# Optimization experiments

Hardware: AMD Instinct MI355X
Metric: run time of the kernel (lower is better)

## Reference

```python
import jax, jax.numpy as jnp
import numpy as np

N, F_IN, H, C, E, K = 100000, 128, 512, 16, 3200000, 3
EPS = 1e-5


def setup_inputs() -> dict:
    key = jax.random.key(0)
    ks = jax.random.split(key, 12)
    x = jax.random.normal(ks[0], (N, F_IN), jnp.float32)
    edge_index = jax.random.randint(ks[1], (2, E), 0, N, jnp.int64)
    # TAGConv has K+1 hop linears (bias folded into one vector, like PyG)
    W1 = jax.random.normal(ks[2], (K + 1, F_IN, H), jnp.float32) * 0.02
    b1 = jnp.zeros((H,), jnp.float32)
    W2 = jax.random.normal(ks[3], (K + 1, H, H), jnp.float32) * 0.02
    b2 = jnp.zeros((H,), jnp.float32)
    W3 = jax.random.normal(ks[4], (K + 1, H, C), jnp.float32) * 0.02
    b3 = jnp.zeros((C,), jnp.float32)
    gn1_w = jnp.ones((H,), jnp.float32)
    gn1_b = jnp.zeros((H,), jnp.float32)
    gn1_a = jnp.ones((H,), jnp.float32)  # mean_scale alpha
    gn2_w = jnp.ones((H,), jnp.float32)
    gn2_b = jnp.zeros((H,), jnp.float32)
    gn2_a = jnp.ones((H,), jnp.float32)
    return {"x": x, "edge_index": edge_index,
            "W1": W1, "b1": b1, "W2": W2, "b2": b2, "W3": W3, "b3": b3,
            "gn1_w": gn1_w, "gn1_b": gn1_b, "gn1_a": gn1_a,
            "gn2_w": gn2_w, "gn2_b": gn2_b, "gn2_a": gn2_a}


def _gcn_norm(edge_index, n):
    # PyG TAGConv: gcn_norm with add_self_loops=False, all-ones edge weights
    row, col = edge_index[0], edge_index[1]  # source j, target i
    deg = jax.ops.segment_sum(jnp.ones((edge_index.shape[1],), jnp.float32), col,
                              num_segments=n)
    dinv = jnp.where(deg > 0, jax.lax.rsqrt(jnp.maximum(deg, 1.0)), 0.0)
    return row, col, dinv[row] * dinv[col]


def _prop(h, row, col, norm, n):
    # out[i] = sum_{(j->i)} norm_e * h[j]
    return jax.ops.segment_sum(norm[:, None] * h[row], col, num_segments=n)


def _tagconv(x, row, col, norm, W, b):
    n = x.shape[0]
    out = x @ W[0]
    h = x
    for k in range(1, W.shape[0]):
        h = _prop(h, row, col, norm, n)
        out = out + h @ W[k]
    return out + b


def _graphnorm(x, w, b, a):
    # single graph: per-graph mean/var over all nodes
    mean = jnp.mean(x, axis=0)
    sub = x - a * mean
    var = jnp.mean(sub * sub, axis=0)
    return sub * jax.lax.rsqrt(var + EPS) * w + b


def reference(x, edge_index, W1, b1, W2, b2, W3, b3,
              gn1_w, gn1_b, gn1_a, gn2_w, gn2_b, gn2_a):
    n = x.shape[0]
    row, col, norm = _gcn_norm(edge_index, n)
    h = jax.nn.relu(_tagconv(x, row, col, norm, W1, b1))
    h = _graphnorm(h, gn1_w, gn1_b, gn1_a)
    h = jax.nn.relu(_tagconv(h, row, col, norm, W2, b2))
    h = _graphnorm(h, gn2_w, gn2_b, gn2_a)
    return _tagconv(h, row, col, norm, W3, b3)
```

## Files before the change

### kernel.cpp

```cpp
#include <hip/hip_runtime.h>

#define NN 100000
#define EE 3200000
#define EPSF 1e-5f

typedef unsigned short u16;
typedef short bf16x8 __attribute__((ext_vector_type(8)));
typedef float f32x4 __attribute__((ext_vector_type(4)));

static inline int cdiv(int a, int b) { return (a + b - 1) / b; }

__device__ __forceinline__ float b2f(u16 u) {
    return __uint_as_float((unsigned int)u << 16);
}
__device__ __forceinline__ u16 f2b(float f) {
    unsigned int i = __float_as_uint(f);
    return (u16)((i + 0x7FFFu + ((i >> 16) & 1u)) >> 16);
}
__device__ __forceinline__ int ep_src(unsigned int p) { return (int)(p & 0x1FFFFu); }
__device__ __forceinline__ float ep_w(unsigned int p) {
    return __uint_as_float(p & 0xFFFE0000u);
}
__device__ __forceinline__ unsigned pkhi(float f0, float f1) {
    return __builtin_amdgcn_perm(__float_as_uint(f1), __float_as_uint(f0), 0x07060302u);
}

__global__ void k_init(int* __restrict__ deg, int* __restrict__ cursor,
                       float* __restrict__ stats) {
    int i = blockIdx.x * 256 + threadIdx.x;
    if (i < NN) {
        deg[i] = 0;
        cursor[i] = 0;
    }
    if (i < 2048) stats[i] = 0.f;
}

__global__ void k_deg(const int* __restrict__ col, int* __restrict__ deg) {
    int i = blockIdx.x * 256 + threadIdx.x;
    if (i < EE) atomicAdd(&deg[col[i]], 1);
}

__global__ void k_dinv(const int* __restrict__ deg, float* __restrict__ dinv) {
    int i = blockIdx.x * 256 + threadIdx.x;
    if (i < NN) {
        int d = deg[i];
        dinv[i] = d > 0 ? rsqrtf((float)d) : 0.f;
    }
}

__global__ void k_scan(const int* __restrict__ deg, int* __restrict__ offs) {
    __shared__ int sh[1024];
    int tid = threadIdx.x;
    int start = tid * 98;
    int end = min(start + 98, NN);
    int sum = 0;
    for (int i = start; i < end; ++i) sum += deg[i];
    sh[tid] = sum;
    __syncthreads();
    for (int off = 1; off < 1024; off <<= 1) {
        int t = (tid >= off) ? sh[tid - off] : 0;
        __syncthreads();
        sh[tid] += t;
        __syncthreads();
    }
    int base = tid ? sh[tid - 1] : 0;
    for (int i = start; i < end; ++i) {
        offs[i] = base;
        base += deg[i];
    }
    if (tid == 1023) offs[NN] = sh[1023];
}

__global__ void k_scatter(const int* __restrict__ row, const int* __restrict__ col,
                          const float* __restrict__ dinv, const int* __restrict__ offs,
                          int* __restrict__ cursor, unsigned int* __restrict__ ep) {
    int i = blockIdx.x * 256 + threadIdx.x;
    if (i < EE) {
        int c = col[i], r = row[i];
        int pos = offs[c] + atomicAdd(&cursor[c], 1);
        float w = dinv[r] * dinv[c];
        unsigned int u = __float_as_uint(w);
        unsigned int rb = (u + 0xFFFFu + ((u >> 17) & 1u)) & 0xFFFE0000u;
        ep[pos] = rb | (unsigned int)r;
    }
}

__global__ void k_cvt(const float* __restrict__ src, u16* __restrict__ dst, int n4) {
    int idx = blockIdx.x * 256 + threadIdx.x;
    if (idx >= n4) return;
    float4 v = ((const float4*)src)[idx];
    ushort4 o;
    o.x = f2b(v.x);
    o.y = f2b(v.y);
    o.z = f2b(v.z);
    o.w = f2b(v.w);
    ((ushort4*)dst)[idx] = o;
}

__global__ void k_cvt8s(const u16* __restrict__ src, int lds_, unsigned char* __restrict__ dst,
                        int ldd) {
    int idx = blockIdx.x * 256 + threadIdx.x;
    if (idx >= NN * 128) return;
    int node = idx >> 7, f2 = (idx & 127) << 1;
    ushort2 v = *(const ushort2*)(src + (size_t)node * lds_ + f2);
    int pk = __builtin_amdgcn_cvt_pk_fp8_f32(b2f(v.x), b2f(v.y), 0, false);
    uchar2 o;
    o.x = (unsigned char)(pk & 0xFF);
    o.y = (unsigned char)((pk >> 8) & 0xFF);
    *(uchar2*)(dst + (size_t)node * ldd + f2) = o;
}

template <int S8>
__global__ void k_prop_t(const void* __restrict__ in, int ldin,
                         unsigned char* __restrict__ out8, int ldo8,
                         const int* __restrict__ offs, const unsigned int* __restrict__ ep) {
    int node = blockIdx.x;
    int f2 = threadIdx.x << 1;
    int s = offs[node], e = offs[node + 1];
    const u16* inb = (const u16*)in;
    const unsigned char* in8 = (const unsigned char*)in;
    float a0 = 0.f, a1 = 0.f;
    int t = s;
    for (; t + 4 <= e; t += 4) {
        unsigned int p0 = ep[t], p1 = ep[t + 1], p2 = ep[t + 2], p3 = ep[t + 3];
        float x0, y0, x1, y1, x2, y2, x3, y3;
        if (S8) {
            uchar2 c0 = *(const uchar2*)(in8 + (size_t)ep_src(p0) * ldin + f2);
            uchar2 c1 = *(const uchar2*)(in8 + (size_t)ep_src(p1) * ldin + f2);
            uchar2 c2 = *(const uchar2*)(in8 + (size_t)ep_src(p2) * ldin + f2);
            uchar2 c3 = *(const uchar2*)(in8 + (size_t)ep_src(p3) * ldin + f2);
            int w0 = c0.x | (c0.y << 8), w1 = c1.x | (c1.y << 8);
            int w2 = c2.x | (c2.y << 8), w3 = c3.x | (c3.y << 8);
            x0 = __builtin_amdgcn_cvt_f32_fp8(w0, 0);
            y0 = __builtin_amdgcn_cvt_f32_fp8(w0, 1);
            x1 = __builtin_amdgcn_cvt_f32_fp8(w1, 0);
            y1 = __builtin_amdgcn_cvt_f32_fp8(w1, 1);
            x2 = __builtin_amdgcn_cvt_f32_fp8(w2, 0);
            y2 = __builtin_amdgcn_cvt_f32_fp8(w2, 1);
            x3 = __builtin_amdgcn_cvt_f32_fp8(w3, 0);
            y3 = __builtin_amdgcn_cvt_f32_fp8(w3, 1);
        } else {
            ushort2 v0 = *(const ushort2*)(inb + (size_t)ep_src(p0) * ldin + f2);
            ushort2 v1 = *(const ushort2*)(inb + (size_t)ep_src(p1) * ldin + f2);
            ushort2 v2 = *(const ushort2*)(inb + (size_t)ep_src(p2) * ldin + f2);
            ushort2 v3 = *(const ushort2*)(inb + (size_t)ep_src(p3) * ldin + f2);
            x0 = b2f(v0.x);
            y0 = b2f(v0.y);
            x1 = b2f(v1.x);
            y1 = b2f(v1.y);
            x2 = b2f(v2.x);
            y2 = b2f(v2.y);
            x3 = b2f(v3.x);
            y3 = b2f(v3.y);
        }
        float w0 = ep_w(p0), w1 = ep_w(p1), w2 = ep_w(p2), w3 = ep_w(p3);
        a0 = fmaf(w0, x0, a0);
        a1 = fmaf(w0, y0, a1);
        a0 = fmaf(w1, x1, a0);
        a1 = fmaf(w1, y1, a1);
        a0 = fmaf(w2, x2, a0);
        a1 = fmaf(w2, y2, a1);
        a0 = fmaf(w3, x3, a0);
        a1 = fmaf(w3, y3, a1);
    }
    for (; t < e; ++t) {
        unsigned int p0 = ep[t];
        float x0, y0;
        if (S8) {
            uchar2 c0 = *(const uchar2*)(in8 + (size_t)ep_src(p0) * ldin + f2);
            int w = c0.x | (c0.y << 8);
            x0 = __builtin_amdgcn_cvt_f32_fp8(w, 0);
            y0 = __builtin_amdgcn_cvt_f32_fp8(w, 1);
        } else {
            ushort2 v0 = *(const ushort2*)(inb + (size_t)ep_src(p0) * ldin + f2);
            x0 = b2f(v0.x);
            y0 = b2f(v0.y);
        }
        float w0 = ep_w(p0);
        a0 = fmaf(w0, x0, a0);
        a1 = fmaf(w0, y0, a1);
    }
    int pk = __builtin_amdgcn_cvt_pk_fp8_f32(a0, a1, 0, false);
    uchar2 o8;
    o8.x = (unsigned char)(pk & 0xFF);
    o8.y = (unsigned char)((pk >> 8) & 0xFF);
    *(uchar2*)(out8 + (size_t)node * ldo8 + f2) = o8;
}

__global__ void k_prop256(const unsigned char* __restrict__ in, int ldin,
                          unsigned char* __restrict__ out, int ldout,
                          const int* __restrict__ offs, const unsigned int* __restrict__ ep) {
    int node = blockIdx.x;
    int f4 = threadIdx.x << 2;
    int s = offs[node], e = offs[node + 1];
    float a0 = 0, a1 = 0, a2 = 0, a3 = 0;
    int t = s;
    for (; t + 4 <= e; t += 4) {
        unsigned int p[4];
        unsigned int v[4];
#pragma unroll
        for (int u = 0; u < 4; ++u) p[u] = ep[t + u];
#pragma unroll
        for (int u = 0; u < 4; ++u)
            v[u] = *(const unsigned int*)(in + (size_t)ep_src(p[u]) * ldin + f4);
#pragma unroll
        for (int u = 0; u < 4; ++u) {
            float w = ep_w(p[u]);
            a0 = fmaf(w, __builtin_amdgcn_cvt_f32_fp8((int)v[u], 0), a0);
            a1 = fmaf(w, __builtin_amdgcn_cvt_f32_fp8((int)v[u], 1), a1);
            a2 = fmaf(w, __builtin_amdgcn_cvt_f32_fp8((int)v[u], 2), a2);
            a3 = fmaf(w, __builtin_amdgcn_cvt_f32_fp8((int)v[u], 3), a3);
        }
    }
    for (; t < e; ++t) {
        unsigned int p0 = ep[t];
        unsigned int v = *(const unsigned int*)(in + (size_t)ep_src(p0) * ldin + f4);
        float w = ep_w(p0);
        a0 = fmaf(w, __builtin_amdgcn_cvt_f32_fp8((int)v, 0), a0);
        a1 = fmaf(w, __builtin_amdgcn_cvt_f32_fp8((int)v, 1), a1);
        a2 = fmaf(w, __builtin_amdgcn_cvt_f32_fp8((int)v, 2), a2);
        a3 = fmaf(w, __builtin_amdgcn_cvt_f32_fp8((int)v, 3), a3);
    }
    int p01 = __builtin_amdgcn_cvt_pk_fp8_f32(a0, a1, 0, false);
    int p23 = __builtin_amdgcn_cvt_pk_fp8_f32(a2, a3, 0, false);
    unsigned int o = (unsigned)(p01 & 0xFFFF) | ((unsigned)p23 << 16);
    *(unsigned int*)(out + (size_t)node * ldout + f4) = o;
}

__global__ void k_prop16(const float* __restrict__ in, int ldin,
                         const float* __restrict__ add, int ldadd,
                         float* __restrict__ out, const float* __restrict__ bias,
                         const int* __restrict__ offs, const unsigned int* __restrict__ ep) {
    int node = blockIdx.x * 16 + (threadIdx.x >> 4);
    if (node >= NN) return;
    int f = threadIdx.x & 15;
    float acc = add[(size_t)node * ldadd + f];
    int s = offs[node], e = offs[node + 1];
    int t = s;
    for (; t + 8 <= e; t += 8) {
        unsigned int p[8];
        float v[8];
#pragma unroll
        for (int u = 0; u < 8; ++u) p[u] = ep[t + u];
#pragma unroll
        for (int u = 0; u < 8; ++u) v[u] = in[(size_t)ep_src(p[u]) * ldin + f];
#pragma unroll
        for (int u = 0; u < 8; ++u) acc = fmaf(ep_w(p[u]), v[u], acc);
    }
    for (; t < e; ++t) {
        unsigned int p0 = ep[t];
        acc = fmaf(ep_w(p0), in[(size_t)ep_src(p0) * ldin + f], acc);
    }
    if (bias) acc += bias[f];
    out[node * 16 + f] = acc;
}

__global__ __launch_bounds__(256, 4) void k_gemm_mfma(
    const void* __restrict__ A0, int lda0, const void* __restrict__ A1, int lda1,
    const void* __restrict__ A2, int lda2, const void* __restrict__ A3, int lda3, int a8mask,
    const u16* __restrict__ B0, const u16* __restrict__ B1, const u16* __restrict__ B2,
    const u16* __restrict__ B3, int ldb, void* __restrict__ Cv, int ldc, int M, int Ncols,
    int Ktot, int Kq, const float* __restrict__ bias, int relu, int cmode,
    float* __restrict__ statsOut) {
    __shared__ __align__(16) char AsB[2][8192];
    __shared__ __align__(16) char BsB[2][8192];
    __shared__ float sstat[256];
    int tid = threadIdx.x;
    int wave = tid >> 6, lane = tid & 63;
    int quad = lane >> 4, lq = lane & 15;
    int wr = wave >> 1, wc = wave & 1;
    int gx = gridDim.x;
    int nwg = gx * (int)gridDim.y;
    int lin = blockIdx.y * gx + blockIdx.x;
    int xcd = lin & 7, kk8 = lin >> 3;
    int q8 = nwg >> 3, r8 = nwg & 7;
    int wgid = (xcd < r8 ? xcd * (q8 + 1) : r8 * (q8 + 1) + (xcd - r8) * q8) + kk8;
    int m0 = (wgid / gx) * 128, n0 = (wgid % gx) * 128;
    int r = tid >> 1, h = tid & 1;
    int gr = m0 + r;
    if (gr > M - 1) gr = M - 1;
    f32x4 acc[4][4] = {};
    if (statsOut) sstat[tid] = 0.f;

    const int NT = Ktot >> 5;
    const int spm = (Kq >> 5) - 1;
    const int sps = __popc(spm);

    auto loadA = [&](int u, uint4& x0, uint4& x1, int& t8) {
        int sU = u < NT ? u : NT - 1;
        int src = sU >> sps, kk = (sU & spm) << 5;
        const char* Ap = (const char*)(src == 0 ? A0 : src == 1 ? A1 : src == 2 ? A2 : A3);
        int lda = src == 0 ? lda0 : src == 1 ? lda1 : src == 2 ? lda2 : lda3;
        t8 = (a8mask >> src) & 1;
        if (t8) {
            x0 = *(const uint4*)(Ap + (size_t)gr * lda + kk + h * 16);
        } else {
            const char* base = Ap + (size_t)gr * ((size_t)lda * 2) + (size_t)kk * 2 + h * 32;
            x0 = *(const uint4*)base;
            x1 = *(const uint4*)(base + 16);
        }
    };
    auto writeA = [&](int buf, uint4 x0, uint4 x1, int t8) {
        uint4 lo, hi;
        if (t8) {
            lo.x = pkhi(__builtin_amdgcn_cvt_f32_fp8((int)x0.x, 0),
                        __builtin_amdgcn_cvt_f32_fp8((int)x0.x, 1));
            lo.y = pkhi(__builtin_amdgcn_cvt_f32_fp8((int)x0.x, 2),
                        __builtin_amdgcn_cvt_f32_fp8((int)x0.x, 3));
            lo.z = pkhi(__builtin_amdgcn_cvt_f32_fp8((int)x0.y, 0),
                        __builtin_amdgcn_cvt_f32_fp8((int)x0.y, 1));
            lo.w = pkhi(__builtin_amdgcn_cvt_f32_fp8((int)x0.y, 2),
                        __builtin_amdgcn_cvt_f32_fp8((int)x0.y, 3));
            hi.x = pkhi(__builtin_amdgcn_cvt_f32_fp8((int)x0.z, 0),
                        __builtin_amdgcn_cvt_f32_fp8((int)x0.z, 1));
            hi.y = pkhi(__builtin_amdgcn_cvt_f32_fp8((int)x0.z, 2),
                        __builtin_amdgcn_cvt_f32_fp8((int)x0.z, 3));
            hi.z = pkhi(__builtin_amdgcn_cvt_f32_fp8((int)x0.w, 0),
                        __builtin_amdgcn_cvt_f32_fp8((int)x0.w, 1));
            hi.w = pkhi(__builtin_amdgcn_cvt_f32_fp8((int)x0.w, 2),
                        __builtin_amdgcn_cvt_f32_fp8((int)x0.w, 3));
        } else {
            lo = x0;
            hi = x1;
        }
        int s = ((r >> 1) & 3) << 4;
        char* dst = AsB[buf] + r * 64;
        *(uint4*)(dst + ((h * 32) ^ s)) = lo;
        *(uint4*)(dst + ((h * 32 + 16) ^ s)) = hi;
    };
    auto stageB = [&](int buf, int u) {
        int sU = u < NT ? u : NT - 1;
        int src = sU >> sps, kk = (sU & spm) << 5;
        const u16* Bp = src == 0 ? B0 : src == 1 ? B1 : src == 2 ? B2 : B3;
#pragma unroll
        for (int i = 0; i < 2; ++i) {
            int L = i * 4096 + wave * 1024 + lane * 16;
            int rr = L >> 6;
            int kog = (L & 63) ^ (((rr >> 1) & 3) << 4);
            int gn = n0 + rr;
            if (gn > Ncols - 1) gn = Ncols - 1;
            const char* g = (const char*)Bp + (size_t)gn * ((size_t)ldb * 2) +
                            (size_t)kk * 2 + kog;
            __builtin_amdgcn_global_load_lds(
                (const __attribute__((address_space(1))) void*)g,
                (__attribute__((address_space(3))) void*)(BsB[buf] + i * 4096 + wave * 1024),
                16, 0, 0);
        }
    };

    uint4 pa0, pa1;
    int pt8;
    {
        uint4 a0_, a1_;
        int t8_;
        loadA(0, a0_, a1_, t8_);
        stageB(0, 0);
        asm volatile("s_waitcnt vmcnt(2)" ::: "memory");
        __builtin_amdgcn_sched_barrier(0);
        writeA(0, a0_, a1_, t8_);
        loadA(1, pa0, pa1, pt8);
        if (pt8)
            asm volatile("s_waitcnt vmcnt(1) lgkmcnt(0)" ::: "memory");
        else
            asm volatile("s_waitcnt vmcnt(2) lgkmcnt(0)" ::: "memory");
        __builtin_amdgcn_sched_barrier(0);
        __builtin_amdgcn_s_barrier();
    }

    int cur = 0;
    for (int t = 0; t < NT; ++t) {
        int nxt = cur ^ 1;
        stageB(nxt, t + 1);
        const char* Ac = AsB[cur];
        const char* Bc = BsB[cur];
        bf16x8 af[4], bfr[4];
#pragma unroll
        for (int i = 0; i < 4; ++i) {
            int rr = wr * 64 + i * 16 + lq;
            af[i] = *(const bf16x8*)(Ac + rr * 64 + ((quad * 16) ^ (((rr >> 1) & 3) << 4)));
        }
#pragma unroll
        for (int j = 0; j < 4; ++j) {
            int nn2 = wc * 64 + j * 16 + lq;
            bfr[j] = *(const bf16x8*)(Bc + nn2 * 64 + ((quad * 16) ^ (((nn2 >> 1) & 3) << 4)));
        }
#pragma unroll
        for (int i = 0; i < 4; ++i)
#pragma unroll
            for (int j = 0; j < 4; ++j)
                acc[i][j] = __builtin_amdgcn_mfma_f32_16x16x32_bf16(af[i], bfr[j], acc[i][j],
                                                                    0, 0, 0);
        asm volatile("s_waitcnt vmcnt(2)" ::: "memory");
        __builtin_amdgcn_sched_barrier(0);
        writeA(nxt, pa0, pa1, pt8);
        loadA(t + 2, pa0, pa1, pt8);
        if (pt8)
            asm volatile("s_waitcnt vmcnt(1) lgkmcnt(0)" ::: "memory");
        else
            asm volatile("s_waitcnt vmcnt(2) lgkmcnt(0)" ::: "memory");
        __builtin_amdgcn_sched_barrier(0);
        __builtin_amdgcn_s_barrier();
        cur = nxt;
    }

#pragma unroll
    for (int i = 0; i < 4; ++i) {
#pragma unroll
        for (int j = 0; j < 4; ++j) {
            int jc = wc * 64 + j * 16 + lq;
            int c = n0 + jc;
            bool cok = c < Ncols;
            float bcol = (bias && cok) ? bias[c] : 0.f;
            int rbase = m0 + wr * 64 + i * 16 + quad * 4;
            float ls = 0.f, lq2 = 0.f;
#pragma unroll
            for (int reg = 0; reg < 4; ++reg) {
                int rr = rbase + reg;
                if (rr >= M || !cok) continue;
                float t = acc[i][j][reg];
                if (cmode == 2) t += b2f(*((u16*)Cv + (size_t)rr * ldc + c));
                t += bcol;
                if (relu) t = fmaxf(t, 0.f);
                if (cmode == 0)
                    ((float*)Cv)[(size_t)rr * ldc + c] = t;
                else
                    *((u16*)Cv + (size_t)rr * ldc + c) = f2b(t);
                ls += t;
                lq2 += t * t;
            }
            if (statsOut && cok) {
                atomicAdd(&sstat[jc], ls);
                atomicAdd(&sstat[128 + jc], lq2);
            }
        }
    }
    if (statsOut) {
        __syncthreads();
        if (tid < 128)
            atomicAdd(&statsOut[n0 + tid], sstat[tid]);
        else
            atomicAdd(&statsOut[512 + n0 + (tid - 128)], sstat[tid]);
    }
}

__global__ void k_gnorm(u16* __restrict__ X, int ld, const float* __restrict__ stats,
                        const float* __restrict__ w, const float* __restrict__ b,
                        const float* __restrict__ a) {
    int i = blockIdx.x;
    int c = threadIdx.x * 2;
    const float invn = 1.f / NN;
    ushort2 v = *(ushort2*)(X + (size_t)i * ld + c);
    float x0 = b2f(v.x), x1 = b2f(v.y);
    {
        float m = stats[c] * invn, q = stats[512 + c] * invn, al = a[c];
        float var = q - (2.f * al - al * al) * m * m;
        x0 = (x0 - al * m) * rsqrtf(var + EPSF) * w[c] + b[c];
    }
    {
        int c1 = c + 1;
        float m = stats[c1] * invn, q = stats[512 + c1] * invn, al = a[c1];
        float var = q - (2.f * al - al * al) * m * m;
        x1 = (x1 - al * m) * rsqrtf(var + EPSF) * w[c1] + b[c1];
    }
    v.x = f2b(x0);
    v.y = f2b(x1);
    *(ushort2*)(X + (size_t)i * ld + c) = v;
}

__global__ void k_wt(const float* __restrict__ src, u16* __restrict__ dst, int I, int O,
                     int total) {
    int idx = blockIdx.x * 256 + threadIdx.x;
    if (idx >= total) return;
    int io = I * O;
    int k = idx / io, rem = idx - k * io;
    int n = rem / I, i = rem - n * I;
    dst[idx] = f2b(src[(size_t)k * io + (size_t)i * O + n]);
}

__global__ void k_wt3(const float* __restrict__ W3, u16* __restrict__ W3T) {
    int idx = blockIdx.x * 256 + threadIdx.x;
    if (idx >= 64 * 512) return;
    int n = idx >> 9, i = idx & 511;
    int k = n >> 4, f = n & 15;
    W3T[idx] = f2b(W3[((size_t)k * 512 + i) * 16 + f]);
}

extern "C" void kernel_launch(void* const* d_in, const int* in_sizes, int n_in,
                              void* d_out, int out_size, void* d_ws, size_t ws_size,
                              hipStream_t stream) {
    const float* x = (const float*)d_in[0];
    const int* ei = (const int*)d_in[1];
    const float* W1 = (const float*)d_in[2];
    const float* b1 = (const float*)d_in[3];
    const float* W2 = (const float*)d_in[4];
    const float* b2 = (const float*)d_in[5];
    const float* W3 = (const float*)d_in[6];
    const float* b3 = (const float*)d_in[7];
    const float* g1w = (const float*)d_in[8];
    const float* g1b = (const float*)d_in[9];
    const float* g1a = (const float*)d_in[10];
    const float* g2w = (const float*)d_in[11];
    const float* g2b = (const float*)d_in[12];
    const float* g2a = (const float*)d_in[13];
    const int* row = ei;
    const int* col = ei + EE;

    char* p = (char*)d_ws;
    auto alloc = [&](size_t bytes) {
        char* r = p;
        p += (bytes + 255) & ~(size_t)255;
        return r;
    };
    u16* H1 = (u16*)alloc((size_t)NN * 512 * 2);
    u16* Y = (u16*)alloc((size_t)NN * 512 * 2);
    unsigned char* X8 = (unsigned char*)alloc((size_t)NN * 256);
    unsigned int* ep = (unsigned int*)alloc((size_t)EE * 4);
    u16* W1T = (u16*)alloc((size_t)4 * 512 * 128 * 2);
    u16* W2T = (u16*)alloc((size_t)4 * 512 * 512 * 2);
    u16* W3T = (u16*)alloc(64 * 512 * 2);
    float* dinv = (float*)alloc((size_t)NN * 4);
    float* stats = (float*)alloc(2048 * 4);
    int* deg = (int*)alloc((size_t)NN * 4);
    int* offs = (int*)alloc((size_t)(NN + 1) * 4);
    int* cursor = (int*)alloc((size_t)NN * 4);
    (void)ws_size;
    (void)in_sizes;
    (void)n_in;
    (void)out_size;

    u16* xb = Y;
    unsigned char* F8a = (unsigned char*)Y + (size_t)NN * 256;
    unsigned char* F8b = (unsigned char*)Y + (size_t)NN * 256 + (size_t)NN * 128;

    k_init<<<cdiv(NN, 256), 256, 0, stream>>>(deg, cursor, stats);
    k_deg<<<cdiv(EE, 256), 256, 0, stream>>>(col, deg);
    k_dinv<<<cdiv(NN, 256), 256, 0, stream>>>(deg, dinv);
    k_scan<<<1, 1024, 0, stream>>>(deg, offs);
    k_scatter<<<cdiv(EE, 256), 256, 0, stream>>>(row, col, dinv, offs, cursor, ep);
    k_wt<<<cdiv(4 * 128 * 512, 256), 256, 0, stream>>>(W1, W1T, 128, 512, 4 * 128 * 512);
    k_wt<<<cdiv(4 * 512 * 512, 256), 256, 0, stream>>>(W2, W2T, 512, 512, 4 * 512 * 512);
    k_wt3<<<cdiv(64 * 512, 256), 256, 0, stream>>>(W3, W3T);

    dim3 gg(512 / 128, cdiv(NN, 128));
    const size_t WQ = (size_t)512 * 512;
    const size_t W1Q = (size_t)512 * 128;

    k_cvt<<<cdiv(NN * 32, 256), 256, 0, stream>>>(x, xb, NN * 32);
    k_prop_t<0><<<NN, 64, 0, stream>>>(xb, 128, F8a, 128, offs, ep);
    k_prop_t<1><<<NN, 64, 0, stream>>>(F8a, 128, F8b, 128, offs, ep);
    k_prop_t<1><<<NN, 64, 0, stream>>>(F8b, 128, X8, 128, offs, ep);
    k_gemm_mfma<<<gg, 256, 0, stream>>>(xb, 128, F8a, 128, F8b, 128, X8, 128, 14, W1T,
                                        W1T + W1Q, W1T + 2 * W1Q, W1T + 3 * W1Q, 128, H1, 512,
                                        NN, 512, 512, 128, b1, 1, 1, stats);
    k_gnorm<<<NN, 256, 0, stream>>>(H1, 512, stats, g1w, g1b, g1a);

    unsigned char* hpA = (unsigned char*)H1;
    unsigned char* hpB = (unsigned char*)H1 + 256;
    {
        u16* h1c0 = H1;
        k_cvt8s<<<cdiv(NN * 128, 256), 256, 0, stream>>>(h1c0, 512, X8, 256);
        k_gemm_mfma<<<gg, 256, 0, stream>>>(h1c0, 512, h1c0, 512, h1c0, 512, h1c0, 512, 0,
                                            W2T, W2T, W2T, W2T, 512, Y, 512, NN, 512, 256,
                                            256, nullptr, 0, 1, nullptr);
        k_prop256<<<NN, 64, 0, stream>>>(X8, 256, hpA, 1024, offs, ep);
        k_prop256<<<NN, 64, 0, stream>>>(hpA, 1024, hpB, 1024, offs, ep);
        k_prop256<<<NN, 64, 0, stream>>>(hpB, 1024, X8, 256, offs, ep);
        k_gemm_mfma<<<gg, 256, 0, stream>>>(hpA, 1024, hpB, 1024, X8, 256, X8, 256, 7,
                                            W2T + WQ, W2T + 2 * WQ, W2T + 3 * WQ, W2T, 512,
                                            Y, 512, NN, 512, 768, 256, nullptr, 0, 2,
                                            nullptr);
    }
    {
        u16* h1c1 = H1 + 256;
        k_cvt8s<<<cdiv(NN * 128, 256), 256, 0, stream>>>(h1c1, 512, X8, 256);
        k_prop256<<<NN, 64, 0, stream>>>(X8, 256, hpA, 1024, offs, ep);
        k_prop256<<<NN, 64, 0, stream>>>(hpA, 1024, hpB, 1024, offs, ep);
        k_prop256<<<NN, 64, 0, stream>>>(hpB, 1024, X8, 256, offs, ep);
        k_gemm_mfma<<<gg, 256, 0, stream>>>(h1c1, 512, hpA, 1024, hpB, 1024, X8, 256, 14,
                                            W2T + 256, W2T + WQ + 256, W2T + 2 * WQ + 256,
                                            W2T + 3 * WQ + 256, 512, Y, 512, NN, 512, 1024,
                                            256, b2, 1, 2, stats + 1024);
    }
    k_gnorm<<<NN, 256, 0, stream>>>(Y, 512, stats + 1024, g2w, g2b, g2a);

    float* G = (float*)H1;
    float* tA = (float*)X8;
    float* tB = tA + (size_t)NN * 16;
    {
        dim3 g3(1, cdiv(NN, 128));
        k_gemm_mfma<<<g3, 256, 0, stream>>>(Y, 512, Y, 512, Y, 512, Y, 512, 0, W3T, W3T, W3T,
                                            W3T, 512, G, 64, NN, 64, 512, 512, nullptr, 0, 0,
                                            nullptr);
    }
    k_prop16<<<cdiv(NN, 16), 256, 0, stream>>>(G + 48, 64, G + 32, 64, tA, nullptr, offs, ep);
    k_prop16<<<cdiv(NN, 16), 256, 0, stream>>>(tA, 16, G + 16, 64, tB, nullptr, offs, ep);
    k_prop16<<<cdiv(NN, 16), 256, 0, stream>>>(tB, 16, G + 0, 64, (float*)d_out, b3, offs, ep);
}
```

Measured before the change: 2.988 ms.

## Deepen A-operand prefetch to two tiles and drop XCD-aware block remap

Restructures the MFMA GEMM main loop to prefetch A tiles two iterations ahead, unrolling by two with fixed register sets so that the vmcnt waits are uniform. FP8 A loads are split into two 8-byte loads so that both the FP8 and bf16 paths issue two loads each, and the FP8 write layout is changed to match. The XCD-aware workgroup remapping is removed in favour of plain blockIdx tiling, and launch bounds are lowered to 3 waves per SIMD to leave room for the extra prefetch registers. The deeper prefetch is meant to hide global load latency. In exchange it costs occupancy and L2 locality, and the unrolled loop assumes an even tile count NT.

```diff
diff --git a/kernel.cpp b/kernel.cpp
--- a/kernel.cpp
+++ b/kernel.cpp
@@ -255,7 +255,7 @@
     out[node * 16 + f] = acc;
 }
 
-__global__ __launch_bounds__(256, 4) void k_gemm_mfma(
+__global__ __launch_bounds__(256, 3) void k_gemm_mfma(
     const void* __restrict__ A0, int lda0, const void* __restrict__ A1, int lda1,
     const void* __restrict__ A2, int lda2, const void* __restrict__ A3, int lda3, int a8mask,
     const u16* __restrict__ B0, const u16* __restrict__ B1, const u16* __restrict__ B2,
@@ -269,13 +269,7 @@
     int wave = tid >> 6, lane = tid & 63;
     int quad = lane >> 4, lq = lane & 15;
     int wr = wave >> 1, wc = wave & 1;
-    int gx = gridDim.x;
-    int nwg = gx * (int)gridDim.y;
-    int lin = blockIdx.y * gx + blockIdx.x;
-    int xcd = lin & 7, kk8 = lin >> 3;
-    int q8 = nwg >> 3, r8 = nwg & 7;
-    int wgid = (xcd < r8 ? xcd * (q8 + 1) : r8 * (q8 + 1) + (xcd - r8) * q8) + kk8;
-    int m0 = (wgid / gx) * 128, n0 = (wgid % gx) * 128;
+    int m0 = blockIdx.y * 128, n0 = blockIdx.x * 128;
     int r = tid >> 1, h = tid & 1;
     int gr = m0 + r;
     if (gr > M - 1) gr = M - 1;
@@ -293,7 +287,13 @@
         int lda = src == 0 ? lda0 : src == 1 ? lda1 : src == 2 ? lda2 : lda3;
         t8 = (a8mask >> src) & 1;
         if (t8) {
-            x0 = *(const uint4*)(Ap + (size_t)gr * lda + kk + h * 16);
+            const char* base = Ap + (size_t)gr * lda + kk;
+            uint2 a = *(const uint2*)(base + h * 8);
+            uint2 b = *(const uint2*)(base + 16 + h * 8);
+            x0.x = a.x;
+            x0.y = a.y;
+            x1.x = b.x;
+            x1.y = b.y;
         } else {
             const char* base = Ap + (size_t)gr * ((size_t)lda * 2) + (size_t)kk * 2 + h * 32;
             x0 = *(const uint4*)base;
@@ -301,8 +301,10 @@
         }
     };
     auto writeA = [&](int buf, uint4 x0, uint4 x1, int t8) {
-        uint4 lo, hi;
+        int s = ((r >> 1) & 3) << 4;
+        char* dst = AsB[buf] + r * 64;
         if (t8) {
+            uint4 lo, hi;
             lo.x = pkhi(__builtin_amdgcn_cvt_f32_fp8((int)x0.x, 0),
                         __builtin_amdgcn_cvt_f32_fp8((int)x0.x, 1));
             lo.y = pkhi(__builtin_amdgcn_cvt_f32_fp8((int)x0.x, 2),
@@ -311,22 +313,20 @@
                         __builtin_amdgcn_cvt_f32_fp8((int)x0.y, 1));
             lo.w = pkhi(__builtin_amdgcn_cvt_f32_fp8((int)x0.y, 2),
                         __builtin_amdgcn_cvt_f32_fp8((int)x0.y, 3));
-            hi.x = pkhi(__builtin_amdgcn_cvt_f32_fp8((int)x0.z, 0),
-                        __builtin_amdgcn_cvt_f32_fp8((int)x0.z, 1));
-            hi.y = pkhi(__builtin_amdgcn_cvt_f32_fp8((int)x0.z, 2),
-                        __builtin_amdgcn_cvt_f32_fp8((int)x0.z, 3));
-            hi.z = pkhi(__builtin_amdgcn_cvt_f32_fp8((int)x0.w, 0),
-                        __builtin_amdgcn_cvt_f32_fp8((int)x0.w, 1));
-            hi.w = pkhi(__builtin_amdgcn_cvt_f32_fp8((int)x0.w, 2),
-                        __builtin_amdgcn_cvt_f32_fp8((int)x0.w, 3));
+            hi.x = pkhi(__builtin_amdgcn_cvt_f32_fp8((int)x1.x, 0),
+                        __builtin_amdgcn_cvt_f32_fp8((int)x1.x, 1));
+            hi.y = pkhi(__builtin_amdgcn_cvt_f32_fp8((int)x1.x, 2),
+                        __builtin_amdgcn_cvt_f32_fp8((int)x1.x, 3));
+            hi.z = pkhi(__builtin_amdgcn_cvt_f32_fp8((int)x1.y, 0),
+                        __builtin_amdgcn_cvt_f32_fp8((int)x1.y, 1));
+            hi.w = pkhi(__builtin_amdgcn_cvt_f32_fp8((int)x1.y, 2),
+                        __builtin_amdgcn_cvt_f32_fp8((int)x1.y, 3));
+            *(uint4*)(dst + ((h * 16) ^ s)) = lo;
+            *(uint4*)(dst + ((32 + h * 16) ^ s)) = hi;
         } else {
-            lo = x0;
-            hi = x1;
-        }
-        int s = ((r >> 1) & 3) << 4;
-        char* dst = AsB[buf] + r * 64;
-        *(uint4*)(dst + ((h * 32) ^ s)) = lo;
-        *(uint4*)(dst + ((h * 32 + 16) ^ s)) = hi;
+            *(uint4*)(dst + ((h * 32) ^ s)) = x0;
+            *(uint4*)(dst + ((h * 32 + 16) ^ s)) = x1;
+        }
     };
     auto stageB = [&](int buf, int u) {
         int sU = u < NT ? u : NT - 1;
@@ -347,32 +347,9 @@
                 16, 0, 0);
         }
     };
-
-    uint4 pa0, pa1;
-    int pt8;
-    {
-        uint4 a0_, a1_;
-        int t8_;
-        loadA(0, a0_, a1_, t8_);
-        stageB(0, 0);
-        asm volatile("s_waitcnt vmcnt(2)" ::: "memory");
-        __builtin_amdgcn_sched_barrier(0);
-        writeA(0, a0_, a1_, t8_);
-        loadA(1, pa0, pa1, pt8);
-        if (pt8)
-            asm volatile("s_waitcnt vmcnt(1) lgkmcnt(0)" ::: "memory");
-        else
-            asm volatile("s_waitcnt vmcnt(2) lgkmcnt(0)" ::: "memory");
-        __builtin_amdgcn_sched_barrier(0);
-        __builtin_amdgcn_s_barrier();
-    }
-
-    int cur = 0;
-    for (int t = 0; t < NT; ++t) {
-        int nxt = cur ^ 1;
-        stageB(nxt, t + 1);
-        const char* Ac = AsB[cur];
-        const char* Bc = BsB[cur];
+    auto compute = [&](int bufc) {
+        const char* Ac = AsB[bufc];
+        const char* Bc = BsB[bufc];
         bf16x8 af[4], bfr[4];
 #pragma unroll
         for (int i = 0; i < 4; ++i) {
@@ -390,17 +367,48 @@
             for (int j = 0; j < 4; ++j)
                 acc[i][j] = __builtin_amdgcn_mfma_f32_16x16x32_bf16(af[i], bfr[j], acc[i][j],
                                                                     0, 0, 0);
-        asm volatile("s_waitcnt vmcnt(2)" ::: "memory");
+    };
+
+    uint4 wAx, wAy, wBx, wBy;
+    int wA8, wB8;
+    {
+        uint4 a0x, a0y;
+        int a08;
+        loadA(0, a0x, a0y, a08);
+        stageB(0, 0);
+        loadA(1, wAx, wAy, wA8);
+        loadA(2, wBx, wBy, wB8);
+        asm volatile("s_waitcnt vmcnt(4)" ::: "memory");
         __builtin_amdgcn_sched_barrier(0);
-        writeA(nxt, pa0, pa1, pt8);
-        loadA(t + 2, pa0, pa1, pt8);
-        if (pt8)
-            asm volatile("s_waitcnt vmcnt(1) lgkmcnt(0)" ::: "memory");
-        else
-            asm volatile("s_waitcnt vmcnt(2) lgkmcnt(0)" ::: "memory");
+        writeA(0, a0x, a0y, a08);
+        asm volatile("s_waitcnt lgkmcnt(0)" ::: "memory");
         __builtin_amdgcn_sched_barrier(0);
         __builtin_amdgcn_s_barrier();
-        cur = nxt;
+    }
+
+    for (int t = 0; t < NT; t += 2) {
+        {
+            stageB(1, t + 1);
+            compute(0);
+            asm volatile("s_waitcnt vmcnt(4)" ::: "memory");
+            __builtin_amdgcn_sched_barrier(0);
+            writeA(1, wAx, wAy, wA8);
+            loadA(t + 3, wAx, wAy, wA8);
+            asm volatile("s_waitcnt vmcnt(2) lgkmcnt(0)" ::: "memory");
+            __builtin_amdgcn_sched_barrier(0);
+            __builtin_amdgcn_s_barrier();
+        }
+        {
+            stageB(0, t + 2);
+            compute(1);
+            asm volatile("s_waitcnt vmcnt(4)" ::: "memory");
+            __builtin_amdgcn_sched_barrier(0);
+            writeA(0, wBx, wBy, wB8);
+            loadA(t + 4, wBx, wBy, wB8);
+            asm volatile("s_waitcnt vmcnt(2) lgkmcnt(0)" ::: "memory");
+            __builtin_amdgcn_sched_barrier(0);
+            __builtin_amdgcn_s_barrier();
+        }
     }
 
 #pragma unroll
```

Result: slower. 3.343 ms (+11.9%).
